# Kernel optimization log

Measured on AMD Instinct MI355X. Metric: run time of the kernel, lower is better.

The kernel has to match this reference:

```python
import jax, jax.numpy as jnp
import numpy as np

B, S, D = 1, 2048, 2048
H, G, HD = 32, 8, 64          # heads, kv groups, head_dim
GS = H // G                   # group size = 4
EPS = 1e-6


def _rmsnorm(v, w):
    vf = v.astype(jnp.float32)
    n = vf * jax.lax.rsqrt(jnp.mean(vf * vf, axis=-1, keepdims=True) + EPS)
    return (n * (1.0 + w.astype(jnp.float32))).astype(v.dtype)


def _rope(v, cos, sin):
    # v: [b, h, s, hd]; cos/sin: [s, hd] (rot_dim == head_dim)
    half = v.shape[-1] // 2
    x1, x2 = v[..., :half], v[..., half:]
    rotated = jnp.concatenate([-x2, x1], axis=-1)
    c = cos[None, None, :, :]
    s = sin[None, None, :, :]
    return (v * c + rotated * s).astype(v.dtype)


def setup_inputs() -> dict:
    key = jax.random.key(0)
    ks = jax.random.split(key, 8)
    x = jax.random.normal(ks[0], (B, S, D), dtype=jnp.float32)
    # causal mask: True above diagonal => masked out
    mask = jnp.triu(jnp.ones((S, S), dtype=bool), k=1)
    # standard RoPE tables, full rotary dim == head_dim
    inv_freq = 1.0 / (10000.0 ** (jnp.arange(0, HD, 2, dtype=jnp.float32) / HD))
    angles = jnp.arange(S, dtype=jnp.float32)[:, None] * inv_freq[None, :]
    angles = jnp.concatenate([angles, angles], axis=-1)  # [S, HD]
    cos = jnp.cos(angles)
    sin = jnp.sin(angles)
    sc = 1.0 / np.sqrt(D)
    Wq = jax.random.normal(ks[1], (2 * H * HD, D), dtype=jnp.float32) * sc
    Wk = jax.random.normal(ks[2], (G * HD, D), dtype=jnp.float32) * sc
    Wv = jax.random.normal(ks[3], (G * HD, D), dtype=jnp.float32) * sc
    Wo = jax.random.normal(ks[4], (D, H * HD), dtype=jnp.float32) * sc
    q_norm_w = jnp.zeros((HD,), dtype=jnp.float32)
    k_norm_w = jnp.zeros((HD,), dtype=jnp.float32)
    return {"x": x, "mask": mask, "cos": cos, "sin": sin, "Wq": Wq,
            "Wk": Wk, "Wv": Wv, "Wo": Wo,
            "q_norm_w": q_norm_w, "k_norm_w": k_norm_w}


def reference(x, mask, cos, sin, Wq, Wk, Wv, Wo, q_norm_w, k_norm_w):
    b, s, _ = x.shape
    d_out = H * HD
    # fused q + gate projection: [b, s, H, 2*HD]
    qg = jnp.einsum('bsd,ed->bse', x, Wq).reshape(b, s, H, 2 * HD)
    q = qg[..., :HD]                         # [b, s, H, HD]
    gate = qg[..., HD:].reshape(b, s, d_out)  # [b, s, d_out]
    k = jnp.einsum('bsd,ed->bse', x, Wk).reshape(b, s, G, HD)
    v = jnp.einsum('bsd,ed->bse', x, Wv).reshape(b, s, G, HD)
    q = q.transpose(0, 2, 1, 3)   # [b, H, s, HD]
    k = k.transpose(0, 2, 1, 3)   # [b, G, s, HD]
    v = v.transpose(0, 2, 1, 3)
    q = _rmsnorm(q, q_norm_w)
    k = _rmsnorm(k, k_norm_w)
    q = _rope(q, cos[:s], sin[:s])
    k = _rope(k, cos[:s], sin[:s])
    # GQA without materializing repeated K/V: group queries as [b, G, GS, s, HD]
    qg_ = q.reshape(b, G, GS, s, HD)
    scores = jnp.einsum('bghqd,bgkd->bghqk', qg_, k)   # [b, G, GS, s, s]
    scores = jnp.where(mask[None, None, None, :s, :s], -jnp.inf, scores)
    scale = HD ** (-0.5)
    w = jax.nn.softmax((scores * scale).astype(jnp.float32), axis=-1).astype(q.dtype)
    ctx = jnp.einsum('bghqk,bgkd->bghqd', w, v)        # [b, G, GS, s, HD]
    ctx = ctx.reshape(b, H, s, HD).transpose(0, 2, 1, 3).reshape(b, s, d_out)
    ctx = ctx * jax.nn.sigmoid(gate)
    return jnp.einsum('bse,de->bsd', ctx, Wo)
```

## Files before the change

### kernel.cpp

```cpp
#include <hip/hip_runtime.h>

typedef __bf16 bf16;
typedef __bf16 bf16x4 __attribute__((ext_vector_type(4)));
typedef __bf16 bf16x8 __attribute__((ext_vector_type(8)));
typedef float f32x4 __attribute__((ext_vector_type(4)));

#define DEV static __device__ __forceinline__

constexpr int S  = 2048;
constexpr int D  = 2048;
constexpr int H  = 32;
constexpr int G  = 8;
constexpr int HD = 64;
constexpr int NQG = 2 * H * HD;
constexpr int LDP = 72;

DEV bf16x8 load8(const bf16* p) { return *reinterpret_cast<const bf16x8*>(p); }

DEV f32x4 mfma16(bf16x8 a, bf16x8 b, f32x4 c) {
  return __builtin_amdgcn_mfma_f32_16x16x32_bf16(a, b, c, 0, 0, 0);
}

DEV void gload_lds16(const bf16* g, bf16* l) {
  __builtin_amdgcn_global_load_lds(
      (const __attribute__((address_space(1))) void*)g,
      (__attribute__((address_space(3))) void*)l, 16, 0, 0);
}

template <int NISS>
DEV void stage_tile(bf16* lds, const bf16* src_row0, size_t ld, int k0, int tid) {
  const int w = tid >> 6, l = tid & 63;
#pragma unroll
  for (int i = 0; i < NISS; ++i) {
    int blk = w * NISS + i;
    int r = blk * 8 + (l >> 3);
    int c = (l & 7) ^ (r & 7);
    gload_lds16(src_row0 + (size_t)r * ld + k0 + c * 8, lds + blk * 512);
  }
}

DEV void stage64_8w(bf16* lds, const bf16* src_row0, size_t ld, int k0, int tid) {
  const int w = tid >> 6, l = tid & 63;
  int r = w * 8 + (l >> 3);
  int c = (l & 7) ^ (r & 7);
  gload_lds16(src_row0 + (size_t)r * ld + k0 + c * 8, lds + w * 512);
}

DEV bf16x8 fragr(const bf16* T, int row, int chunk) {
  return load8(T + row * 64 + (((chunk ^ (row & 7)) << 3)));
}

DEV float fexp2(float x) { return __builtin_amdgcn_exp2f(x); }
DEV float frcp(float x)  { return __builtin_amdgcn_rcpf(x); }

__global__ __launch_bounds__(256) void cvt_all(
    const float* __restrict__ x,  const float* __restrict__ wq,
    const float* __restrict__ wk, const float* __restrict__ wv,
    const float* __restrict__ wo,
    bf16* __restrict__ xb,  bf16* __restrict__ wqb, bf16* __restrict__ wkb,
    bf16* __restrict__ wvb, bf16* __restrict__ wob)
{
  long c = (long)blockIdx.x * 256 + threadIdx.x;
  const float* src; bf16* dst; long off;
  if      (c <  524288) { src = x;  dst = xb;  off = c; }
  else if (c < 1572864) { src = wq; dst = wqb; off = c -  524288; }
  else if (c < 1703936) { src = wk; dst = wkb; off = c - 1572864; }
  else if (c < 1835008) { src = wv; dst = wvb; off = c - 1703936; }
  else                  { src = wo; dst = wob; off = c - 1835008; }
  long i = off * 8;
  const float4* p = reinterpret_cast<const float4*>(src + i);
  float4 a = p[0], b = p[1];
  bf16x8 o;
  o[0] = (bf16)a.x; o[1] = (bf16)a.y; o[2] = (bf16)a.z; o[3] = (bf16)a.w;
  o[4] = (bf16)b.x; o[5] = (bf16)b.y; o[6] = (bf16)b.z; o[7] = (bf16)b.w;
  *reinterpret_cast<bf16x8*>(dst + i) = o;
}

DEV void rms_rope_store(f32x4 acc[4][4], bf16* __restrict__ dst,
                        const float* __restrict__ w,
                        const float* __restrict__ cosb,
                        const float* __restrict__ sinb,
                        int s0, int ln, int hi, float outscale)
{
  float wgt[4];
#pragma unroll
  for (int ni = 0; ni < 4; ++ni) wgt[ni] = 1.0f + w[ni * 16 + ln];
#pragma unroll
  for (int mi = 0; mi < 4; ++mi)
#pragma unroll
    for (int j = 0; j < 4; ++j) {
      int s = s0 + mi * 16 + hi * 4 + j;
      float v0 = acc[mi][0][j], v1 = acc[mi][1][j];
      float v2 = acc[mi][2][j], v3 = acc[mi][3][j];
      float ss = v0 * v0 + v1 * v1 + v2 * v2 + v3 * v3;
      ss += __shfl_xor(ss, 1);
      ss += __shfl_xor(ss, 2);
      ss += __shfl_xor(ss, 4);
      ss += __shfl_xor(ss, 8);
      float inv = __builtin_amdgcn_rsqf(ss * (1.0f / 64.0f) + 1e-6f);
      float xf[4] = {v0 * inv * wgt[0], v1 * inv * wgt[1],
                     v2 * inv * wgt[2], v3 * inv * wgt[3]};
#pragma unroll
      for (int ni = 0; ni < 4; ++ni) {
        int d = ni * 16 + ln;
        float c  = cosb[s * HD + d];
        float sn = sinb[s * HD + d];
        float rot = (ni < 2) ? -xf[ni + 2] : xf[ni - 2];
        dst[(size_t)s * HD + d] = (bf16)((xf[ni] * c + rot * sn) * outscale);
      }
    }
}

__global__ __launch_bounds__(256, 3) void gemm_qkv(
    const bf16* __restrict__ X, const bf16* __restrict__ Wq,
    const bf16* __restrict__ Wk, const bf16* __restrict__ Wv,
    const float* __restrict__ cosb, const float* __restrict__ sinb,
    const float* __restrict__ qw, const float* __restrict__ kw,
    bf16* __restrict__ qg, bf16* __restrict__ qrot,
    bf16* __restrict__ krot, bf16* __restrict__ vt)
{
  __shared__ __align__(16) bf16 As[128 * 64];
  __shared__ __align__(16) bf16 Bs[128 * 64];

  const int tid  = threadIdx.x;
  const int wave = tid >> 6;
  const int lane = tid & 63;
  const int ln = lane & 15, hi = lane >> 4;
  const int wm = wave >> 1, wn = wave & 1;
  const int m0 = blockIdx.y * 128;
  const int nt = blockIdx.x;

  const bf16* W; int n0;
  if (nt < 32)      { W = Wq; n0 = nt * 128; }
  else if (nt < 36) { W = Wk; n0 = (nt - 32) * 128; }
  else              { W = Wv; n0 = (nt - 36) * 128; }

  const bf16* arow = X + (size_t)m0 * D;
  const bf16* brow = W + (size_t)n0 * D;

  f32x4 acc[4][4] = {};

  for (int k0 = 0; k0 < D; k0 += 64) {
    __syncthreads();
    stage_tile<4>(As, arow, D, k0, tid);
    stage_tile<4>(Bs, brow, D, k0, tid);
    __syncthreads();
#pragma unroll
    for (int kk = 0; kk < 64; kk += 32) {
      bf16x8 a[4], b[4];
#pragma unroll
      for (int mi = 0; mi < 4; ++mi) a[mi] = fragr(As, wm * 64 + mi * 16 + ln, (kk >> 3) + hi);
#pragma unroll
      for (int ni = 0; ni < 4; ++ni) b[ni] = fragr(Bs, wn * 64 + ni * 16 + ln, (kk >> 3) + hi);
#pragma unroll
      for (int mi = 0; mi < 4; ++mi)
#pragma unroll
        for (int ni = 0; ni < 4; ++ni)
          acc[mi][ni] = mfma16(a[mi], b[ni], acc[mi][ni]);
    }
  }

  const int s0 = m0 + wm * 64;
  if (nt < 32) {
    if (wn == 0) {
      rms_rope_store(acc, qrot + (size_t)nt * S * HD, qw, cosb, sinb,
                     s0, ln, hi, 0.18033688011111204f);
    } else {
#pragma unroll
      for (int mi = 0; mi < 4; ++mi)
#pragma unroll
        for (int ni = 0; ni < 4; ++ni)
#pragma unroll
          for (int j = 0; j < 4; ++j) {
            int r = s0 + mi * 16 + hi * 4 + j;
            int c = nt * 128 + 64 + ni * 16 + ln;
            qg[(size_t)r * NQG + c] = (bf16)acc[mi][ni][j];
          }
    }
  } else if (nt < 36) {
    int g8 = (nt - 32) * 2 + wn;
    rms_rope_store(acc, krot + (size_t)g8 * S * HD, kw, cosb, sinb,
                   s0, ln, hi, 1.0f);
  } else {
    int nrel = (nt - 36) * 128;
#pragma unroll
    for (int mi = 0; mi < 4; ++mi)
#pragma unroll
      for (int ni = 0; ni < 4; ++ni)
#pragma unroll
        for (int j = 0; j < 4; ++j) {
          int r = s0 + mi * 16 + hi * 4 + j;
          int c = nrel + wn * 64 + ni * 16 + ln;
          vt[(size_t)c * S + r] = (bf16)acc[mi][ni][j];
        }
  }
}

__global__ __launch_bounds__(256, 3) void gemm_out(
    const bf16* __restrict__ A, const bf16* __restrict__ W,
    float* __restrict__ C)
{
  __shared__ __align__(16) bf16 As[128 * 64];
  __shared__ __align__(16) bf16 Bs[128 * 64];

  const int tid  = threadIdx.x;
  const int wave = tid >> 6;
  const int lane = tid & 63;
  const int ln = lane & 15, hi = lane >> 4;
  const int wm = wave >> 1, wn = wave & 1;
  const int m0 = blockIdx.y * 128;
  const int n0 = blockIdx.x * 128;

  const bf16* arow = A + (size_t)m0 * D;
  const bf16* brow = W + (size_t)n0 * D;

  f32x4 acc[4][4] = {};

  for (int k0 = 0; k0 < D; k0 += 64) {
    __syncthreads();
    stage_tile<4>(As, arow, D, k0, tid);
    stage_tile<4>(Bs, brow, D, k0, tid);
    __syncthreads();
#pragma unroll
    for (int kk = 0; kk < 64; kk += 32) {
      bf16x8 a[4], b[4];
#pragma unroll
      for (int mi = 0; mi < 4; ++mi) a[mi] = fragr(As, wm * 64 + mi * 16 + ln, (kk >> 3) + hi);
#pragma unroll
      for (int ni = 0; ni < 4; ++ni) b[ni] = fragr(Bs, wn * 64 + ni * 16 + ln, (kk >> 3) + hi);
#pragma unroll
      for (int mi = 0; mi < 4; ++mi)
#pragma unroll
        for (int ni = 0; ni < 4; ++ni)
          acc[mi][ni] = mfma16(a[mi], b[ni], acc[mi][ni]);
    }
  }

#pragma unroll
  for (int mi = 0; mi < 4; ++mi)
#pragma unroll
    for (int ni = 0; ni < 4; ++ni)
#pragma unroll
      for (int j = 0; j < 4; ++j) {
        int r = m0 + wm * 64 + mi * 16 + hi * 4 + j;
        int c = n0 + wn * 64 + ni * 16 + ln;
        C[(size_t)r * D + c] = acc[mi][ni][j];
      }
}

#define BARRIER() asm volatile("s_barrier" ::: "memory")
#define VMDRAIN() asm volatile("s_waitcnt vmcnt(0)" ::: "memory")

DEV void attn_phase(const bf16* __restrict__ qrot, const bf16* __restrict__ krow,
                    const bf16* __restrict__ vrow, const bf16* __restrict__ qg,
                    bf16* __restrict__ ctxg,
                    bf16* Kb0, bf16* Kb1, bf16* Vb0, bf16* Vb1, bf16* pw,
                    int h, int qchunk, int nt, int ln, int hi, int tid)
{
  const int qb = qchunk * 64 + ((tid >> 6) & 3) * 16;
  const int q  = qb + ln;

  const bf16* qbase = qrot + ((size_t)h * S + qb + ln) * HD + hi * 8;
  bf16x8 q0 = load8(qbase);
  bf16x8 q1 = load8(qbase + 32);

  f32x4 po[4] = {};
  float m = -INFINITY, l = 0.f;

  stage64_8w(Kb0, krow, 64, 0, tid);
  stage64_8w(Vb0, vrow, S, 0, tid);
  VMDRAIN();
  BARRIER();

  int cur = 0;
  for (int t = 0; t < nt; ++t) {
    const bf16* Kb = cur ? Kb1 : Kb0;
    const bf16* Vb = cur ? Vb1 : Vb0;

    if (t + 1 < nt) {
      bf16* Kn = cur ? Kb0 : Kb1;
      bf16* Vn = cur ? Vb0 : Vb1;
      stage64_8w(Kn, krow + (size_t)(t + 1) * 64 * 64, 64, 0, tid);
      stage64_8w(Vn, vrow, S, (t + 1) * 64, tid);
    }

    bf16x8 kf0[4], kf1[4];
#pragma unroll
    for (int kr = 0; kr < 4; ++kr) {
      kf0[kr] = fragr(Kb, kr * 16 + ln, hi);
      kf1[kr] = fragr(Kb, kr * 16 + ln, hi + 4);
    }
    bf16x8 bv0[4], bv1[4];
#pragma unroll
    for (int dt = 0; dt < 4; ++dt) {
      bv0[dt] = fragr(Vb, dt * 16 + ln, hi);
      bv1[dt] = fragr(Vb, dt * 16 + ln, hi + 4);
    }

    f32x4 sc[4] = {};
    __builtin_amdgcn_s_setprio(1);
#pragma unroll
    for (int kr = 0; kr < 4; ++kr) {
      sc[kr] = mfma16(kf0[kr], q0, sc[kr]);
      sc[kr] = mfma16(kf1[kr], q1, sc[kr]);
    }
    __builtin_amdgcn_s_setprio(0);

    float pmax = -INFINITY;
    if (t == nt - 1) {
      const int key0 = t << 6;
#pragma unroll
      for (int kr = 0; kr < 4; ++kr)
#pragma unroll
        for (int j = 0; j < 4; ++j) {
          int key = key0 + kr * 16 + hi * 4 + j;
          float v = (key <= q) ? sc[kr][j] : -INFINITY;
          sc[kr][j] = v;
          pmax = fmaxf(pmax, v);
        }
    } else {
#pragma unroll
      for (int kr = 0; kr < 4; ++kr)
#pragma unroll
        for (int j = 0; j < 4; ++j) pmax = fmaxf(pmax, sc[kr][j]);
    }
    pmax = fmaxf(pmax, __shfl_xor(pmax, 16));
    pmax = fmaxf(pmax, __shfl_xor(pmax, 32));

    if (__any(pmax > m + 8.0f)) {
      float mn = fmaxf(m, pmax);
      float c  = fexp2(m - mn);
      l *= c;
      float cc[4];
#pragma unroll
      for (int j = 0; j < 4; ++j) cc[j] = __shfl(c, hi * 4 + j);
#pragma unroll
      for (int dt = 0; dt < 4; ++dt)
#pragma unroll
        for (int j = 0; j < 4; ++j) po[dt][j] *= cc[j];
      m = mn;
    }

    float ps = 0.f;
#pragma unroll
    for (int kr = 0; kr < 4; ++kr)
#pragma unroll
      for (int j = 0; j < 4; ++j) {
        float e = fexp2(sc[kr][j] - m);
        sc[kr][j] = e;
        ps += e;
      }
    ps += __shfl_xor(ps, 16);
    ps += __shfl_xor(ps, 32);
    l += ps;

#pragma unroll
    for (int kr = 0; kr < 4; ++kr) {
      unsigned w0, w1;
      asm("v_cvt_pk_bf16_f32 %0, %1, %2" : "=v"(w0) : "v"(sc[kr][0]), "v"(sc[kr][1]));
      asm("v_cvt_pk_bf16_f32 %0, %1, %2" : "=v"(w1) : "v"(sc[kr][2]), "v"(sc[kr][3]));
      uint2 w = {w0, w1};
      *reinterpret_cast<uint2*>(pw + ln * LDP + kr * 16 + hi * 4) = w;
    }
    bf16x8 pa0 = load8(pw + ln * LDP + hi * 8);
    bf16x8 pa1 = load8(pw + ln * LDP + 32 + hi * 8);

    __builtin_amdgcn_s_setprio(1);
#pragma unroll
    for (int dt = 0; dt < 4; ++dt) {
      po[dt] = mfma16(pa0, bv0[dt], po[dt]);
      po[dt] = mfma16(pa1, bv1[dt], po[dt]);
    }
    __builtin_amdgcn_s_setprio(0);

    VMDRAIN();
    BARRIER();
    cur ^= 1;
  }

  float lf[4];
#pragma unroll
  for (int j = 0; j < 4; ++j) lf[j] = __shfl(l, hi * 4 + j);
#pragma unroll
  for (int dt = 0; dt < 4; ++dt)
#pragma unroll
    for (int j = 0; j < 4; ++j) {
      int qq = qb + hi * 4 + j;
      int d  = dt * 16 + ln;
      float o  = po[dt][j] * frcp(lf[j]);
      float gv = (float)qg[(size_t)qq * NQG + h * 128 + 64 + d];
      float sg = frcp(1.0f + fexp2(gv * -1.442695040888963f));
      ctxg[(size_t)qq * D + h * 64 + d] = (bf16)(o * sg);
    }
}

__global__ __launch_bounds__(512) void attn(
    const bf16* __restrict__ qrot, const bf16* __restrict__ krot,
    const bf16* __restrict__ vt, const bf16* __restrict__ qg,
    bf16* __restrict__ ctxg)
{
  __shared__ __align__(16) bf16 Kbuf[2][64 * 64];
  __shared__ __align__(16) bf16 Vbuf[2][64 * 64];
  __shared__ __align__(16) bf16 Pl[8][16 * LDP];

  const int tid  = threadIdx.x;
  const int lane = tid & 63;
  const int ln = lane & 15, hi = lane >> 4;

  const int bid = blockIdx.x;
  const int g   = bid & 7;
  const int i   = bid >> 3;
  const int hp  = i & 1;
  const int pr  = i >> 1;
  const int h   = g * 4 + hp * 2 + ((tid >> 6) >> 2);
  bf16* pw = &Pl[tid >> 6][0];

  const bf16* krow = krot + (size_t)g * S * HD;
  const bf16* vrow = vt + (size_t)g * 64 * S;

  attn_phase(qrot, krow, vrow, qg, ctxg,
             &Kbuf[0][0], &Kbuf[1][0], &Vbuf[0][0], &Vbuf[1][0], pw,
             h, pr, pr + 1, ln, hi, tid);
  attn_phase(qrot, krow, vrow, qg, ctxg,
             &Kbuf[0][0], &Kbuf[1][0], &Vbuf[0][0], &Vbuf[1][0], pw,
             h, 31 - pr, 32 - pr, ln, hi, tid);
}

extern "C" void kernel_launch(void* const* d_in, const int* in_sizes, int n_in,
                              void* d_out, int out_size, void* d_ws, size_t ws_size,
                              hipStream_t stream) {
  const float* x    = (const float*)d_in[0];
  const float* cosb = (const float*)d_in[2];
  const float* sinb = (const float*)d_in[3];
  const float* Wq   = (const float*)d_in[4];
  const float* Wk   = (const float*)d_in[5];
  const float* Wv   = (const float*)d_in[6];
  const float* Wo   = (const float*)d_in[7];
  const float* qw   = (const float*)d_in[8];
  const float* kw   = (const float*)d_in[9];

  char* ws = (char*)d_ws;
  bf16* xb   = (bf16*)(ws);
  bf16* Wqb  = (bf16*)(ws + ( 8u << 20));
  bf16* Wkb  = (bf16*)(ws + (24u << 20));
  bf16* Wvb  = (bf16*)(ws + (26u << 20));
  bf16* Wob  = (bf16*)(ws + (28u << 20));
  bf16* qg   = (bf16*)(ws + (36u << 20));
  bf16* vt   = (bf16*)(ws + (54u << 20));
  bf16* qrot = (bf16*)(ws + (56u << 20));
  bf16* krot = (bf16*)(ws + (64u << 20));
  bf16* ctxg = (bf16*)(ws + (66u << 20));
  float* out = (float*)d_out;

  cvt_all<<<dim3(9216), 256, 0, stream>>>(x, Wq, Wk, Wv, Wo,
                                          xb, Wqb, Wkb, Wvb, Wob);

  gemm_qkv<<<dim3(40, 16), 256, 0, stream>>>(xb, Wqb, Wkb, Wvb,
                                             cosb, sinb, qw, kw,
                                             qg, qrot, krot, vt);
  attn<<<dim3(256), 512, 0, stream>>>(qrot, krot, vt, qg, ctxg);
  gemm_out<<<dim3(16, 16), 256, 0, stream>>>(ctxg, Wob, out);
}
```

Measured before the change: 145.3 us.

## Double-buffer LDS tiles in QKV and output GEMMs to overlap loads with MFMA

Both projection GEMMs now use two LDS buffers per operand and prefetch the next K-tile with global_load_lds while computing the current one, with a single drain-and-barrier per iteration instead of two syncs. MFMA sections are wrapped in s_setprio to favour math waves. The doubled LDS footprint lowers the occupancy hint from 3 to 2 blocks per CU, which may reduce latency hiding across blocks.

Result: slower. 166.4 us (+14.5%).

```diff
diff --git a/kernel.cpp b/kernel.cpp
--- a/kernel.cpp
+++ b/kernel.cpp
@@ -26,6 +26,9 @@
       (const __attribute__((address_space(1))) void*)g,
       (__attribute__((address_space(3))) void*)l, 16, 0, 0);
 }
+
+#define BARRIER() asm volatile("s_barrier" ::: "memory")
+#define VMDRAIN() asm volatile("s_waitcnt vmcnt(0)" ::: "memory")
 
 template <int NISS>
 DEV void stage_tile(bf16* lds, const bf16* src_row0, size_t ld, int k0, int tid) {
@@ -111,7 +114,7 @@
     }
 }
 
-__global__ __launch_bounds__(256, 3) void gemm_qkv(
+__global__ __launch_bounds__(256, 2) void gemm_qkv(
     const bf16* __restrict__ X, const bf16* __restrict__ Wq,
     const bf16* __restrict__ Wk, const bf16* __restrict__ Wv,
     const float* __restrict__ cosb, const float* __restrict__ sinb,
@@ -119,8 +122,8 @@
     bf16* __restrict__ qg, bf16* __restrict__ qrot,
     bf16* __restrict__ krot, bf16* __restrict__ vt)
 {
-  __shared__ __align__(16) bf16 As[128 * 64];
-  __shared__ __align__(16) bf16 Bs[128 * 64];
+  __shared__ __align__(16) bf16 As[2][128 * 64];
+  __shared__ __align__(16) bf16 Bs[2][128 * 64];
 
   const int tid  = threadIdx.x;
   const int wave = tid >> 6;
@@ -140,24 +143,37 @@
 
   f32x4 acc[4][4] = {};
 
+  stage_tile<4>(As[0], arow, D, 0, tid);
+  stage_tile<4>(Bs[0], brow, D, 0, tid);
+  VMDRAIN();
+  BARRIER();
+
+  int cur = 0;
   for (int k0 = 0; k0 < D; k0 += 64) {
-    __syncthreads();
-    stage_tile<4>(As, arow, D, k0, tid);
-    stage_tile<4>(Bs, brow, D, k0, tid);
-    __syncthreads();
+    if (k0 + 64 < D) {
+      stage_tile<4>(As[cur ^ 1], arow, D, k0 + 64, tid);
+      stage_tile<4>(Bs[cur ^ 1], brow, D, k0 + 64, tid);
+    }
+    const bf16* Asc = As[cur];
+    const bf16* Bsc = Bs[cur];
 #pragma unroll
     for (int kk = 0; kk < 64; kk += 32) {
       bf16x8 a[4], b[4];
 #pragma unroll
-      for (int mi = 0; mi < 4; ++mi) a[mi] = fragr(As, wm * 64 + mi * 16 + ln, (kk >> 3) + hi);
-#pragma unroll
-      for (int ni = 0; ni < 4; ++ni) b[ni] = fragr(Bs, wn * 64 + ni * 16 + ln, (kk >> 3) + hi);
+      for (int mi = 0; mi < 4; ++mi) a[mi] = fragr(Asc, wm * 64 + mi * 16 + ln, (kk >> 3) + hi);
+#pragma unroll
+      for (int ni = 0; ni < 4; ++ni) b[ni] = fragr(Bsc, wn * 64 + ni * 16 + ln, (kk >> 3) + hi);
+      __builtin_amdgcn_s_setprio(1);
 #pragma unroll
       for (int mi = 0; mi < 4; ++mi)
 #pragma unroll
         for (int ni = 0; ni < 4; ++ni)
           acc[mi][ni] = mfma16(a[mi], b[ni], acc[mi][ni]);
-    }
+      __builtin_amdgcn_s_setprio(0);
+    }
+    VMDRAIN();
+    BARRIER();
+    cur ^= 1;
   }
 
   const int s0 = m0 + wm * 64;
@@ -196,12 +212,12 @@
   }
 }
 
-__global__ __launch_bounds__(256, 3) void gemm_out(
+__global__ __launch_bounds__(256, 2) void gemm_out(
     const bf16* __restrict__ A, const bf16* __restrict__ W,
     float* __restrict__ C)
 {
-  __shared__ __align__(16) bf16 As[128 * 64];
-  __shared__ __align__(16) bf16 Bs[128 * 64];
+  __shared__ __align__(16) bf16 As[2][128 * 64];
+  __shared__ __align__(16) bf16 Bs[2][128 * 64];
 
   const int tid  = threadIdx.x;
   const int wave = tid >> 6;
@@ -216,24 +232,37 @@
 
   f32x4 acc[4][4] = {};
 
+  stage_tile<4>(As[0], arow, D, 0, tid);
+  stage_tile<4>(Bs[0], brow, D, 0, tid);
+  VMDRAIN();
+  BARRIER();
+
+  int cur = 0;
   for (int k0 = 0; k0 < D; k0 += 64) {
-    __syncthreads();
-    stage_tile<4>(As, arow, D, k0, tid);
-    stage_tile<4>(Bs, brow, D, k0, tid);
-    __syncthreads();
+    if (k0 + 64 < D) {
+      stage_tile<4>(As[cur ^ 1], arow, D, k0 + 64, tid);
+      stage_tile<4>(Bs[cur ^ 1], brow, D, k0 + 64, tid);
+    }
+    const bf16* Asc = As[cur];
+    const bf16* Bsc = Bs[cur];
 #pragma unroll
     for (int kk = 0; kk < 64; kk += 32) {
       bf16x8 a[4], b[4];
 #pragma unroll
-      for (int mi = 0; mi < 4; ++mi) a[mi] = fragr(As, wm * 64 + mi * 16 + ln, (kk >> 3) + hi);
-#pragma unroll
-      for (int ni = 0; ni < 4; ++ni) b[ni] = fragr(Bs, wn * 64 + ni * 16 + ln, (kk >> 3) + hi);
+      for (int mi = 0; mi < 4; ++mi) a[mi] = fragr(Asc, wm * 64 + mi * 16 + ln, (kk >> 3) + hi);
+#pragma unroll
+      for (int ni = 0; ni < 4; ++ni) b[ni] = fragr(Bsc, wn * 64 + ni * 16 + ln, (kk >> 3) + hi);
+      __builtin_amdgcn_s_setprio(1);
 #pragma unroll
       for (int mi = 0; mi < 4; ++mi)
 #pragma unroll
         for (int ni = 0; ni < 4; ++ni)
           acc[mi][ni] = mfma16(a[mi], b[ni], acc[mi][ni]);
-    }
+      __builtin_amdgcn_s_setprio(0);
+    }
+    VMDRAIN();
+    BARRIER();
+    cur ^= 1;
   }
 
 #pragma unroll
@@ -247,9 +276,6 @@
         C[(size_t)r * D + c] = acc[mi][ni][j];
       }
 }
-
-#define BARRIER() asm volatile("s_barrier" ::: "memory")
-#define VMDRAIN() asm volatile("s_waitcnt vmcnt(0)" ::: "memory")
 
 DEV void attn_phase(const bf16* __restrict__ qrot, const bf16* __restrict__ krow,
                     const bf16* __restrict__ vrow, const bf16* __restrict__ qg,
```
